# Optimization experiments

Hardware: AMD Instinct MI355X
Metric: run time of the kernel (lower is better)

## Reference

```python
import jax, jax.numpy as jnp
import numpy as np

NGRAM = 16
SUB = 512  # bytes per sub-block


def byte2image(block, ngram=NGRAM):
    """block: (B, L) int -> (B, 1, ngram*8, L-ngram) float32 in [-1, 1]."""
    B, L = block.shape
    blk = block.astype(jnp.int32)
    # nxt[:, i] = blk[:, i+1], last column zero
    nxt = jnp.concatenate([blk[:, 1:], jnp.zeros((B, 1), jnp.int32)], axis=1)
    # 8 bit-shifted views of the byte stream
    shifts = jnp.stack(
        [((blk << s) & 255) + ((nxt >> (8 - s)) & 255) for s in range(8)],
        axis=1,
    )  # (B, 8, L)
    flat = shifts.reshape(B, -1)  # (B, 8*L)
    parts = [flat] + [jnp.roll(flat, -i, axis=1) for i in range(1, ngram)]
    stacked = jnp.concatenate(parts, axis=1).reshape(B, ngram * 8, L)
    result = stacked[:, :, :-ngram].astype(jnp.float32)
    result = (result / 255.0 - 0.5) / 0.5
    return result[:, None]  # (B, 1, ngram*8, L-ngram)


def byte2image_4k(block, ngram=NGRAM):
    """block: (B, 4096) -> (B, 8, ngram*8, 512-ngram)."""
    return jnp.concatenate(
        [byte2image(block[:, i * SUB:(i + 1) * SUB], ngram) for i in range(8)],
        axis=1,
    )


def setup_inputs() -> dict:
    key = jax.random.key(0)
    kx, kw = jax.random.split(key)
    x = jax.random.randint(kx, (256, 4096), 0, 256, dtype=jnp.int64)
    W = jax.random.normal(kw, (496, 64), dtype=jnp.float32) * 0.02
    return {"x": x, "W": W}


def reference(x, W):
    # ByteFormerWrapper.forward with block_size=4096: byte2image_4k then the
    # (opaque) model; model stood in by a linear head over the image width.
    img = byte2image_4k(x)                      # (B, 8, 128, 496)
    out = jnp.einsum('bchw,wo->bcho', img, W)   # (B, 8, 128, 64)
    return out
```

## Files before the change

### kernel.cpp

```cpp
#include <hip/hip_runtime.h>

typedef unsigned short u16;
typedef unsigned int u32;
typedef __attribute__((ext_vector_type(8))) short short8;
typedef _Float16 half8 __attribute__((ext_vector_type(8)));
typedef __attribute__((ext_vector_type(4))) float floatx4;

#define LSTRIDE 72

__global__ __launch_bounds__(256, 4) void byteformer_fused(
    const int* __restrict__ x, const float* __restrict__ Wm,
    float* __restrict__ out) {
  __shared__ __align__(16) u16 As[128 * LSTRIDE];
  __shared__ __align__(16) u16 Bs[128 * LSTRIDE];
  __shared__ float part[256];
  __shared__ float csum[64];

  const int t = threadIdx.x;
  const int mtile = blockIdx.x;
  const int n0 = blockIdx.y * 128;
  const int p0 = 2 * blockIdx.y;

  const int wave = t >> 6, lane = t & 63;
  const int wm = wave >> 1, wn = wave & 1;
  const int quad = lane >> 4, l16 = lane & 15;

  const int sA_sub = t >> 4;
  const int sA_kg  = (t >> 1) & 7;
  const int sA_qh  = t & 1;
  const long xrow = ((long)mtile * 16 + sA_sub) * 512;

  const int sB_o = lane;

  floatx4 acc[4][4];
  #pragma unroll
  for (int mt = 0; mt < 4; ++mt)
    #pragma unroll
    for (int nt = 0; nt < 4; ++nt)
      acc[mt][nt] = floatx4{0.f, 0.f, 0.f, 0.f};

  float csum_local = 0.0f;

  for (int kc = 0; kc < 8; ++kc) {
    const int k0 = kc * 64;
    __syncthreads();

    {
      const int base = k0 + sA_kg * 8;
      int4 a0 = *(const int4*)&x[xrow + base];
      int4 a1 = *(const int4*)&x[xrow + base + 4];
      int c8 = (base + 8 < 512) ? x[xrow + base + 8] : 0;
      int c[9] = {a0.x, a0.y, a0.z, a0.w, a1.x, a1.y, a1.z, a1.w, c8};
      u32 w16[8];
      #pragma unroll
      for (int j = 0; j < 8; ++j) w16[j] = ((u32)c[j] << 8) | (u32)c[j + 1];
      #pragma unroll
      for (int qi = 0; qi < 4; ++qi) {
        const int q = sA_qh * 4 + qi;
        const int sh = 8 - q;
        u32 d[4];
        #pragma unroll
        for (int jp = 0; jp < 4; ++jp) {
          u32 v0 = (w16[2 * jp] >> sh) & 255u;
          u32 v1 = (w16[2 * jp + 1] >> sh) & 255u;
          d[jp] = v0 | (v1 << 16) | 0x64006400u;
        }
        *(u32*)&As[(sA_sub * 8 + q) * LSTRIDE + sA_kg * 8 + 0] = d[0];
        *(u32*)&As[(sA_sub * 8 + q) * LSTRIDE + sA_kg * 8 + 2] = d[1];
        *(u32*)&As[(sA_sub * 8 + q) * LSTRIDE + sA_kg * 8 + 4] = d[2];
        *(u32*)&As[(sA_sub * 8 + q) * LSTRIDE + sA_kg * 8 + 6] = d[3];
      }
    }

    {
      const int cbase = k0 + 16 * wave - p0 - 1;
      float f[17];
      u16 h[17];
      #pragma unroll
      for (int j = 0; j < 17; ++j) {
        int c = cbase + j;
        float v = (c >= 0 && c < 496) ? Wm[c * 64 + sB_o] : 0.0f;
        f[j] = v;
        h[j] = (u16)__builtin_bit_cast(unsigned short, (_Float16)v);
      }
      #pragma unroll
      for (int j = 1; j <= 16; ++j) csum_local += f[j];
      #pragma unroll
      for (int g = 0; g < 2; ++g) {
        const int mgrp = 2 * wave + g;
        #pragma unroll
        for (int pp = 0; pp < 2; ++pp) {
          const int jb = g * 8 + 1 - pp;
          u32 d[4];
          #pragma unroll
          for (int di = 0; di < 4; ++di)
            d[di] = (u32)h[jb + 2 * di] | ((u32)h[jb + 2 * di + 1] << 16);
          u32* dst = (u32*)&Bs[(pp * 64 + sB_o) * LSTRIDE + mgrp * 8];
          dst[0] = d[0]; dst[1] = d[1]; dst[2] = d[2]; dst[3] = d[3];
        }
      }
    }
    __syncthreads();

    #pragma unroll
    for (int ks = 0; ks < 2; ++ks) {
      const int koff = ks * 32 + quad * 8;
      half8 af[4], bf[4];
      #pragma unroll
      for (int mt = 0; mt < 4; ++mt)
        af[mt] = *(const half8*)&As[(wm * 64 + mt * 16 + l16) * LSTRIDE + koff];
      #pragma unroll
      for (int nt = 0; nt < 4; ++nt)
        bf[nt] = *(const half8*)&Bs[(wn * 64 + nt * 16 + l16) * LSTRIDE + koff];
      #pragma unroll
      for (int mt = 0; mt < 4; ++mt)
        #pragma unroll
        for (int nt = 0; nt < 4; ++nt)
          acc[mt][nt] = __builtin_amdgcn_mfma_f32_16x16x32_f16(
              af[mt], bf[nt], acc[mt][nt], 0, 0, 0);
    }
  }

  part[t] = csum_local;
  __syncthreads();
  if (t < 64)
    csum[t] = part[t] + part[t + 64] + part[t + 128] + part[t + 192];
  __syncthreads();

  const float S = 2.0f / 255.0f;
  const float K1 = 1024.0f * S + 1.0f;
  #pragma unroll
  for (int nt = 0; nt < 4; ++nt) {
    int n = n0 + wn * 64 + nt * 16 + l16;
    int p = n >> 6, o = n & 63;
    float cs = K1 * csum[o];
    #pragma unroll
    for (int mt = 0; mt < 4; ++mt) {
      int mbase = mtile * 128 + wm * 64 + mt * 16 + quad * 4;
      #pragma unroll
      for (int i = 0; i < 4; ++i) {
        int mr = mbase + i;
        int bid = mr >> 3, q = mr & 7;
        out[(long)bid * 8192 + (p * 8 + q) * 64 + o] = S * acc[mt][nt][i] - cs;
      }
    }
  }
}

extern "C" void kernel_launch(void* const* d_in, const int* in_sizes, int n_in,
                              void* d_out, int out_size, void* d_ws, size_t ws_size,
                              hipStream_t stream) {
  const int* x = (const int*)d_in[0];
  const float* Wm = (const float*)d_in[1];
  float* out = (float*)d_out;
  byteformer_fused<<<dim3(128, 8), dim3(256), 0, stream>>>(x, Wm, out);
}
```

Measured before the change: 103.0 us.

## Prefetch next K-chunk into registers during MFMA and vectorize LDS stores

Restructures the K loop as a software pipeline: global loads of the byte stream and W for chunk kc+1 are issued into registers before the MFMAs for chunk kc, then written to LDS after a barrier. The aim is to hide global memory latency behind compute. It also replaces per-element fp16 casts with packed cvt_pkrtz conversions, widens LDS stores to 128-bit, and reorders the epilogue loops. The prefetch registers add pressure, so launch bounds drop from 4 to 3 blocks per CU, which lowers occupancy.

```diff
diff --git a/kernel.cpp b/kernel.cpp
--- a/kernel.cpp
+++ b/kernel.cpp
@@ -2,13 +2,18 @@
 
 typedef unsigned short u16;
 typedef unsigned int u32;
-typedef __attribute__((ext_vector_type(8))) short short8;
 typedef _Float16 half8 __attribute__((ext_vector_type(8)));
+typedef __fp16 fp16x2 __attribute__((ext_vector_type(2)));
 typedef __attribute__((ext_vector_type(4))) float floatx4;
 
 #define LSTRIDE 72
 
-__global__ __launch_bounds__(256, 4) void byteformer_fused(
+__device__ __forceinline__ u32 pkrtz(float lo, float hi) {
+  fp16x2 h = __builtin_amdgcn_cvt_pkrtz(lo, hi);
+  return __builtin_bit_cast(u32, h);
+}
+
+__global__ __launch_bounds__(256, 3) void byteformer_fused(
     const int* __restrict__ x, const float* __restrict__ Wm,
     float* __restrict__ out) {
   __shared__ __align__(16) u16 As[128 * LSTRIDE];
@@ -29,7 +34,6 @@
   const int sA_kg  = (t >> 1) & 7;
   const int sA_qh  = t & 1;
   const long xrow = ((long)mtile * 16 + sA_sub) * 512;
-
   const int sB_o = lane;
 
   floatx4 acc[4][4];
@@ -41,66 +45,65 @@
 
   float csum_local = 0.0f;
 
+  int4 a0, a1; int c8; float f[17];
+
+  auto loadG = [&](int kc, int4& A0, int4& A1, int& C8, float (&F)[17]) {
+    const int base = kc * 64 + sA_kg * 8;
+    A0 = *(const int4*)&x[xrow + base];
+    A1 = *(const int4*)&x[xrow + base + 4];
+    C8 = (base + 8 < 512) ? x[xrow + base + 8] : 0;
+    const int cb = kc * 64 + 16 * wave - p0 - 1;
+    #pragma unroll
+    for (int j = 0; j < 17; ++j) {
+      int c = cb + j;
+      F[j] = (c >= 0 && c < 496) ? Wm[c * 64 + sB_o] : 0.0f;
+    }
+  };
+
+  auto writeLDS = [&]() {
+    int c[9] = {a0.x, a0.y, a0.z, a0.w, a1.x, a1.y, a1.z, a1.w, c8};
+    u32 w16[8];
+    #pragma unroll
+    for (int j = 0; j < 8; ++j) w16[j] = ((u32)c[j] << 8) | (u32)c[j + 1];
+    #pragma unroll
+    for (int qi = 0; qi < 4; ++qi) {
+      const int q = sA_qh * 4 + qi;
+      const int sh = 8 - q;
+      u32 d[4];
+      #pragma unroll
+      for (int jp = 0; jp < 4; ++jp) {
+        u32 v0 = (w16[2 * jp] >> sh) & 255u;
+        u32 v1 = (w16[2 * jp + 1] >> sh) & 255u;
+        d[jp] = v0 | (v1 << 16) | 0x64006400u;
+      }
+      *(uint4*)&As[(sA_sub * 8 + q) * LSTRIDE + sA_kg * 8] =
+          uint4{d[0], d[1], d[2], d[3]};
+    }
+    u32 pe[8], po[8];
+    #pragma unroll
+    for (int i = 0; i < 8; ++i) {
+      pe[i] = pkrtz(f[2 * i], f[2 * i + 1]);
+      po[i] = pkrtz(f[2 * i + 1], f[2 * i + 2]);
+    }
+    #pragma unroll
+    for (int g = 0; g < 2; ++g) {
+      const int mgrp = 2 * wave + g;
+      *(uint4*)&Bs[(0 * 64 + sB_o) * LSTRIDE + mgrp * 8] =
+          uint4{po[g * 4], po[g * 4 + 1], po[g * 4 + 2], po[g * 4 + 3]};
+      *(uint4*)&Bs[(1 * 64 + sB_o) * LSTRIDE + mgrp * 8] =
+          uint4{pe[g * 4], pe[g * 4 + 1], pe[g * 4 + 2], pe[g * 4 + 3]};
+    }
+    #pragma unroll
+    for (int j = 1; j <= 16; ++j) csum_local += f[j];
+  };
+
+  loadG(0, a0, a1, c8, f);
+  writeLDS();
+  __syncthreads();
+
   for (int kc = 0; kc < 8; ++kc) {
-    const int k0 = kc * 64;
-    __syncthreads();
-
-    {
-      const int base = k0 + sA_kg * 8;
-      int4 a0 = *(const int4*)&x[xrow + base];
-      int4 a1 = *(const int4*)&x[xrow + base + 4];
-      int c8 = (base + 8 < 512) ? x[xrow + base + 8] : 0;
-      int c[9] = {a0.x, a0.y, a0.z, a0.w, a1.x, a1.y, a1.z, a1.w, c8};
-      u32 w16[8];
-      #pragma unroll
-      for (int j = 0; j < 8; ++j) w16[j] = ((u32)c[j] << 8) | (u32)c[j + 1];
-      #pragma unroll
-      for (int qi = 0; qi < 4; ++qi) {
-        const int q = sA_qh * 4 + qi;
-        const int sh = 8 - q;
-        u32 d[4];
-        #pragma unroll
-        for (int jp = 0; jp < 4; ++jp) {
-          u32 v0 = (w16[2 * jp] >> sh) & 255u;
-          u32 v1 = (w16[2 * jp + 1] >> sh) & 255u;
-          d[jp] = v0 | (v1 << 16) | 0x64006400u;
-        }
-        *(u32*)&As[(sA_sub * 8 + q) * LSTRIDE + sA_kg * 8 + 0] = d[0];
-        *(u32*)&As[(sA_sub * 8 + q) * LSTRIDE + sA_kg * 8 + 2] = d[1];
-        *(u32*)&As[(sA_sub * 8 + q) * LSTRIDE + sA_kg * 8 + 4] = d[2];
-        *(u32*)&As[(sA_sub * 8 + q) * LSTRIDE + sA_kg * 8 + 6] = d[3];
-      }
-    }
-
-    {
-      const int cbase = k0 + 16 * wave - p0 - 1;
-      float f[17];
-      u16 h[17];
-      #pragma unroll
-      for (int j = 0; j < 17; ++j) {
-        int c = cbase + j;
-        float v = (c >= 0 && c < 496) ? Wm[c * 64 + sB_o] : 0.0f;
-        f[j] = v;
-        h[j] = (u16)__builtin_bit_cast(unsigned short, (_Float16)v);
-      }
-      #pragma unroll
-      for (int j = 1; j <= 16; ++j) csum_local += f[j];
-      #pragma unroll
-      for (int g = 0; g < 2; ++g) {
-        const int mgrp = 2 * wave + g;
-        #pragma unroll
-        for (int pp = 0; pp < 2; ++pp) {
-          const int jb = g * 8 + 1 - pp;
-          u32 d[4];
-          #pragma unroll
-          for (int di = 0; di < 4; ++di)
-            d[di] = (u32)h[jb + 2 * di] | ((u32)h[jb + 2 * di + 1] << 16);
-          u32* dst = (u32*)&Bs[(pp * 64 + sB_o) * LSTRIDE + mgrp * 8];
-          dst[0] = d[0]; dst[1] = d[1]; dst[2] = d[2]; dst[3] = d[3];
-        }
-      }
-    }
-    __syncthreads();
+    int4 na0, na1; int nc8; float nf[17];
+    if (kc < 7) loadG(kc + 1, na0, na1, nc8, nf);
 
     #pragma unroll
     for (int ks = 0; ks < 2; ++ks) {
@@ -119,6 +122,14 @@
           acc[mt][nt] = __builtin_amdgcn_mfma_f32_16x16x32_f16(
               af[mt], bf[nt], acc[mt][nt], 0, 0, 0);
     }
+    __syncthreads();
+    if (kc < 7) {
+      a0 = na0; a1 = na1; c8 = nc8;
+      #pragma unroll
+      for (int j = 0; j < 17; ++j) f[j] = nf[j];
+      writeLDS();
+      __syncthreads();
+    }
   }
 
   part[t] = csum_local;
@@ -129,20 +140,21 @@
 
   const float S = 2.0f / 255.0f;
   const float K1 = 1024.0f * S + 1.0f;
+  const int p = p0 + wn;
+  float cs[4];
   #pragma unroll
-  for (int nt = 0; nt < 4; ++nt) {
-    int n = n0 + wn * 64 + nt * 16 + l16;
-    int p = n >> 6, o = n & 63;
-    float cs = K1 * csum[o];
+  for (int nt = 0; nt < 4; ++nt) cs[nt] = K1 * csum[nt * 16 + l16];
+  #pragma unroll
+  for (int mt = 0; mt < 4; ++mt) {
+    int mbase = mtile * 128 + wm * 64 + mt * 16 + quad * 4;
     #pragma unroll
-    for (int mt = 0; mt < 4; ++mt) {
-      int mbase = mtile * 128 + wm * 64 + mt * 16 + quad * 4;
+    for (int i = 0; i < 4; ++i) {
+      int mr = mbase + i;
+      int bid = mr >> 3, q = mr & 7;
+      float* orow = out + (long)bid * 8192 + (p * 8 + q) * 64;
       #pragma unroll
-      for (int i = 0; i < 4; ++i) {
-        int mr = mbase + i;
-        int bid = mr >> 3, q = mr & 7;
-        out[(long)bid * 8192 + (p * 8 + q) * 64 + o] = S * acc[mt][nt][i] - cs;
-      }
+      for (int nt = 0; nt < 4; ++nt)
+        orow[nt * 16 + l16] = S * acc[mt][nt][i] - cs[nt];
     }
   }
 }
```

After: 105.3 us. 2.3% more time.
